# Performance work log

Measured on AMD Instinct MI355X. Metric: run time of the kernel, lower is better.

Reference implementation:

```python
import jax, jax.numpy as jnp
import numpy as np

DIM = 1024
NUM_HEADS = 16
HEAD_DIM = DIM // NUM_HEADS
SCALE = HEAD_DIM ** -0.5
B, N = 4, 2048


def setup_inputs() -> dict:
    key = jax.random.key(0)
    ks = jax.random.split(key, 8)
    s = DIM ** -0.5
    x = jax.random.normal(ks[0], (B, N, DIM), dtype=jnp.float32)
    mask = jax.random.randint(ks[1], (B, N, N), 0, 2, dtype=jnp.int32)
    wq = jax.random.normal(ks[2], (DIM, DIM), dtype=jnp.float32) * s
    wk = jax.random.normal(ks[3], (DIM, DIM), dtype=jnp.float32) * s
    wv = jax.random.normal(ks[4], (DIM, DIM), dtype=jnp.float32) * s
    wp = jax.random.normal(ks[5], (DIM, DIM), dtype=jnp.float32) * s
    bp = jnp.zeros((DIM,), dtype=jnp.float32)
    return {"x": x, "mask": mask, "wq": wq, "wk": wk, "wv": wv, "wp": wp, "bp": bp}


def reference(x, mask, wq, wk, wv, wp, bp):
    Bn, Nn, C = x.shape
    # torch Linear: y = x @ W^T; split heads -> (B, H, N, hd)
    def split_heads(y):
        return y.reshape(Bn, Nn, NUM_HEADS, HEAD_DIM).transpose(0, 2, 1, 3)
    q = split_heads(x @ wq.T)
    k = split_heads(x @ wk.T)
    v = split_heads(x @ wv.T)
    attn = jnp.einsum('bhqd,bhkd->bhqk', q, k) * SCALE  # (B,H,N,N)
    # mask==0 -> -inf; mask is (B,N,N), broadcast over heads
    attn = jnp.where(mask[:, None, :, :] == 0, -jnp.inf, attn)
    attn = jax.nn.softmax(attn, axis=-1)
    out = jnp.einsum('bhqk,bhkd->bhqd', attn, v)  # (B,H,N,hd)
    out = out.transpose(0, 2, 1, 3).reshape(Bn, Nn, C)
    return out @ wp.T + bp
```

## Files before the change

### kernel.cpp

```cpp
#include <hip/hip_runtime.h>
#include <stdint.h>

#define DIM 1024
#define NH 16
#define HD 64
#define BB 4
#define SS 2048
#define MR (BB*SS)
#define QSCALE 0.125f
#define L2E 1.44269504f

typedef float f32x4 __attribute__((ext_vector_type(4)));
typedef float f32x16 __attribute__((ext_vector_type(16)));
typedef __bf16 bf16x8 __attribute__((ext_vector_type(8)));
typedef uint32_t u32x4 __attribute__((ext_vector_type(4)));

typedef __attribute__((address_space(3))) void lds_void;
typedef __attribute__((address_space(1))) void glob_void;
#define GLL16(gp, lp) __builtin_amdgcn_global_load_lds((glob_void*)(gp), (lds_void*)(lp), 16, 0, 0)

static __device__ __forceinline__ ushort f2bf(float f) {
  uint32_t u = __builtin_bit_cast(uint32_t, f);
  u += 0x7FFF + ((u >> 16) & 1);
  return (ushort)(u >> 16);
}

static __device__ __forceinline__ f32x16 mfma32(bf16x8 a, bf16x8 b, f32x16 c) {
  return __builtin_amdgcn_mfma_f32_32x32x16_bf16(a, b, c, 0, 0, 0);
}
static __device__ __forceinline__ uint32_t cvtpk(float lo, float hi) {
  uint32_t r;
  asm("v_cvt_pk_bf16_f32 %0, %1, %2" : "=v"(r) : "v"(lo), "v"(hi));
  return r;
}
static __device__ __forceinline__ void plswap(uint32_t &a, uint32_t &b) {
  asm("v_permlane32_swap_b32 %0, %1" : "+v"(a), "+v"(b));
}

__global__ void cvt_bf16(const float* __restrict__ in, ushort* __restrict__ out,
                         const int n4) {
  const int stride = gridDim.x * blockDim.x;
  for (int i = blockIdx.x * blockDim.x + threadIdx.x; i < n4; i += stride) {
    const float4 v = reinterpret_cast<const float4*>(in)[i];
    ushort4 o;
    o.x = f2bf(v.x); o.y = f2bf(v.y); o.z = f2bf(v.z); o.w = f2bf(v.w);
    reinterpret_cast<ushort4*>(out)[i] = o;
  }
}

__global__ void cvt_w4(const float* __restrict__ w0, const float* __restrict__ w1,
                       const float* __restrict__ w2, const float* __restrict__ w3,
                       ushort* __restrict__ out) {
  const int n4 = DIM * DIM;
  const int rsz = DIM * DIM / 4;
  const int stride = gridDim.x * blockDim.x;
  for (int i = blockIdx.x * blockDim.x + threadIdx.x; i < n4; i += stride) {
    const int r = i / rsz, j = i - r * rsz;
    const float* src = (r == 0) ? w0 : (r == 1) ? w1 : (r == 2) ? w2 : w3;
    const float sc = (r == 0) ? (QSCALE * L2E) : 1.0f;
    const float4 v = reinterpret_cast<const float4*>(src)[j];
    ushort4 o;
    o.x = f2bf(v.x * sc); o.y = f2bf(v.y * sc);
    o.z = f2bf(v.z * sc); o.w = f2bf(v.w * sc);
    reinterpret_cast<ushort4*>(out)[i] = o;
  }
}

__global__ void pack_mask(const int* __restrict__ m, uint32_t* __restrict__ bits,
                          const int npairs) {
  const int lane = threadIdx.x & 63;
  const int wid = (blockIdx.x * blockDim.x + threadIdx.x) >> 6;
  const int nw = (gridDim.x * blockDim.x) >> 6;
  for (int p = wid; p < npairs; p += nw) {
    const int v = m[(size_t)p * 64 + lane];
    const unsigned long long bal = __ballot(v != 0);
    if (lane == 0) reinterpret_cast<unsigned long long*>(bits)[p] = bal;
  }
}

template<int EPI>
__global__ __launch_bounds__(256)
void gemm128(const ushort* __restrict__ A, const ushort* __restrict__ Bm,
             const int N, const int K,
             ushort* __restrict__ q_out, ushort* __restrict__ k_out,
             ushort* __restrict__ vt_out,
             const float* __restrict__ bias, float* __restrict__ c_out) {
  __shared__ __align__(16) ushort As[128 * 64];
  __shared__ __align__(16) ushort Bs[128 * 64];
  const int tid = threadIdx.x;
  const int lane = tid & 63, w = tid >> 6;
  const int l31 = lane & 31, hi = lane >> 5;
  const int gx = gridDim.x;
  int lin = blockIdx.y * gx + blockIdx.x;
  const int qch = (gx * gridDim.y) >> 3;
  lin = (lin & 7) * qch + (lin >> 3);
  const int tm = (lin / gx) * 128;
  const int tn = (lin % gx) * 128;
  const int wm = (w >> 1) * 64;
  const int wn = (w & 1) * 64;

  f32x16 acc[2][2] = {};

  const int srow = w * 32 + (lane >> 3);
  const int scol = ((lane & 7) ^ (lane >> 3)) * 8;
  const ushort* aptr = A + (size_t)(tm + srow) * K + scol;
  const ushort* bptr = Bm + (size_t)(tn + srow) * K + scol;
  ushort* lA = As + (size_t)(w * 32) * 64;
  ushort* lB = Bs + (size_t)(w * 32) * 64;

  const int swr = l31 & 7;

  for (int k0 = 0; k0 < K; k0 += 64) {
#pragma unroll
    for (int it = 0; it < 4; ++it) {
      GLL16(aptr + k0 + (size_t)(it * 8) * K, lA + it * 8 * 64);
      GLL16(bptr + k0 + (size_t)(it * 8) * K, lB + it * 8 * 64);
    }
    __syncthreads();
    bf16x8 af[4][2], bfr[4][2];
#pragma unroll
    for (int kk = 0; kk < 4; ++kk) {
      const int slot = (2 * kk + hi) ^ swr;
#pragma unroll
      for (int t = 0; t < 2; ++t) {
        af[kk][t]  = *reinterpret_cast<const bf16x8*>(As + (wm + t * 32 + l31) * 64 + slot * 8);
        bfr[kk][t] = *reinterpret_cast<const bf16x8*>(Bs + (wn + t * 32 + l31) * 64 + slot * 8);
      }
    }
#pragma unroll
    for (int kk = 0; kk < 4; ++kk)
#pragma unroll
      for (int ti = 0; ti < 2; ++ti)
#pragma unroll
        for (int tj = 0; tj < 2; ++tj)
          acc[ti][tj] = mfma32(af[kk][ti], bfr[kk][tj], acc[ti][tj]);
    __syncthreads();
  }

  if constexpr (EPI == 0) {
    const int which = tn >> 10;
    if (which < 2) {
      ushort* dst = which ? k_out : q_out;
#pragma unroll
      for (int ti = 0; ti < 2; ++ti)
#pragma unroll
        for (int tj = 0; tj < 2; ++tj) {
          const int cc = (tn + wn + tj * 32) & (DIM - 1);
          const int h = cc >> 6, d0 = cc & 63;
          const int mrb = tm + wm + ti * 32;
          const int bb = mrb >> 11, tokb = mrb & (SS - 1);
          const size_t bh = (size_t)bb * NH + h;
#pragma unroll
          for (int r = 0; r < 16; ++r) {
            const int tok = tokb + (r & 3) + 8 * (r >> 2) + 4 * hi;
            dst[(bh * SS + tok) * HD + d0 + l31] = f2bf(acc[ti][tj][r]);
          }
        }
    } else {
      ushort* ws = As + w * 1152;
#pragma unroll
      for (int ti = 0; ti < 2; ++ti)
#pragma unroll
        for (int tj = 0; tj < 2; ++tj) {
          const int cc = (tn + wn + tj * 32) & (DIM - 1);
          const int h = cc >> 6, d0 = cc & 63;
          const int mrb = tm + wm + ti * 32;
          const int bb = mrb >> 11, tokb = mrb & (SS - 1);
          const size_t bh = (size_t)bb * NH + h;
#pragma unroll
          for (int r = 0; r < 16; ++r)
            ws[l31 * 36 + (r & 3) + 8 * (r >> 2) + 4 * hi] = f2bf(acc[ti][tj][r]);
          asm volatile("s_waitcnt lgkmcnt(0)" ::: "memory");
          __builtin_amdgcn_sched_barrier(0);
#pragma unroll
          for (int p = 0; p < 8; ++p) {
            const int dl = p * 4 + (lane >> 4);
            const int tokl = (lane & 15) * 2;
            const uint32_t vv = *reinterpret_cast<const uint32_t*>(ws + dl * 36 + tokl);
            *reinterpret_cast<uint32_t*>(
                vt_out + (bh * HD + d0 + dl) * SS + tokb + tokl) = vv;
          }
          asm volatile("s_waitcnt lgkmcnt(0)" ::: "memory");
          __builtin_amdgcn_sched_barrier(0);
        }
    }
  } else {
#pragma unroll
    for (int ti = 0; ti < 2; ++ti)
#pragma unroll
      for (int tj = 0; tj < 2; ++tj) {
        const int nc = tn + wn + tj * 32 + l31;
#pragma unroll
        for (int r = 0; r < 16; ++r) {
          const int mrow = tm + wm + ti * 32 + (r & 3) + 8 * (r >> 2) + 4 * hi;
          c_out[(size_t)mrow * N + nc] = acc[ti][tj][r] + bias[nc];
        }
      }
  }
}

__global__ __launch_bounds__(512)
void attn_kernel(const ushort* __restrict__ Q, const ushort* __restrict__ Kg,
                 const ushort* __restrict__ Vt, const uint32_t* __restrict__ mb,
                 ushort* __restrict__ O) {
  __shared__ __align__(16) ushort lds[16384];
  __shared__ float rl_lds[8][32];

  const int tid = threadIdx.x, lane = tid & 63, w = tid >> 6;
  const int l31 = lane & 31, hi = lane >> 5;
  const int d = blockIdx.x;
  const int g = d & 63, m = d >> 6;
  const int h = g & 15, b = g >> 4;
  const size_t bh = (size_t)b * NH + h;
  const int q0w = m * 256 + w * 32;
  const int qg = q0w + l31;

  bf16x8 qf[4];
  const ushort* qp = Q + (bh * SS + qg) * HD + hi * 8;
#pragma unroll
  for (int kk = 0; kk < 4; ++kk)
    qf[kk] = *reinterpret_cast<const bf16x8*>(qp + kk * 16);

  f32x16 oacc[2] = {};
  float lrun = 0.f;

  const ushort* kbase = Kg + bh * SS * HD;
  const ushort* vbase = Vt + bh * HD * SS;
  const uint32_t* mrow = mb + ((size_t)b * SS + qg) * (SS / 32);

  auto stage = [&](int buf, int kv0) {
    GLL16(kbase + (size_t)(kv0 + (w >> 2) * 32 + l31) * HD + (w & 3) * 16 + hi * 8,
          lds + buf * 8192 + w * 512);
    GLL16(vbase + (size_t)((w & 1) * 32 + l31) * SS + kv0 + (w >> 1) * 16 + hi * 8,
          lds + buf * 8192 + 4096 + w * 512);
  };

  stage(0, 0);
  uint2 mw = *reinterpret_cast<const uint2*>(mrow);
  int cur = 0;

  for (int kv0 = 0; kv0 < SS; kv0 += 64) {
    __syncthreads();
    uint2 mw_n = mw;
    if (kv0 + 64 < SS) {
      stage(cur ^ 1, kv0 + 64);
      mw_n = *reinterpret_cast<const uint2*>(mrow + ((kv0 + 64) >> 5));
    }

    const ushort* kf = lds + cur * 8192 + lane * 8;
    const ushort* vf = lds + cur * 8192 + 4096 + lane * 8;

    f32x16 st[2];
    __builtin_amdgcn_s_setprio(1);
#pragma unroll
    for (int t = 0; t < 2; ++t) {
      f32x16 s = {};
#pragma unroll
      for (int kk = 0; kk < 4; ++kk) {
        const bf16x8 kfrag = *reinterpret_cast<const bf16x8*>(kf + (t * 4 + kk) * 512);
        s = mfma32(kfrag, qf[kk], s);
      }
      st[t] = s;
    }
    __builtin_amdgcn_s_setprio(0);

    float p[2][16];
#pragma unroll
    for (int t = 0; t < 2; ++t) {
      const uint32_t wts = (t ? mw.y : mw.x) >> (4 * hi);
#pragma unroll
      for (int r = 0; r < 16; ++r) {
        const int sh = (r & 3) + 8 * (r >> 2);
        const float pe = __builtin_amdgcn_exp2f(((wts >> sh) & 1u) ? st[t][r] : -3e38f);
        p[t][r] = pe;
        lrun += pe;
      }
    }

    bf16x8 PA[4];
#pragma unroll
    for (int t = 0; t < 2; ++t) {
      uint32_t pk[8];
#pragma unroll
      for (int i = 0; i < 8; ++i)
        pk[i] = cvtpk(p[t][2 * i], p[t][2 * i + 1]);
      plswap(pk[0], pk[2]);
      plswap(pk[1], pk[3]);
      plswap(pk[4], pk[6]);
      plswap(pk[5], pk[7]);
      const u32x4 lo = {pk[0], pk[1], pk[2], pk[3]};
      const u32x4 hh = {pk[4], pk[5], pk[6], pk[7]};
      PA[2 * t]     = __builtin_bit_cast(bf16x8, lo);
      PA[2 * t + 1] = __builtin_bit_cast(bf16x8, hh);
    }

    __builtin_amdgcn_s_setprio(1);
#pragma unroll
    for (int c = 0; c < 4; ++c)
#pragma unroll
      for (int dt = 0; dt < 2; ++dt) {
        const bf16x8 vfrag = *reinterpret_cast<const bf16x8*>(vf + (c * 2 + dt) * 512);
        oacc[dt] = mfma32(PA[c], vfrag, oacc[dt]);
      }
    __builtin_amdgcn_s_setprio(0);

    mw = mw_n;
    cur ^= 1;
  }

  lrun += __shfl_xor(lrun, 32, 64);
  const float rl = 1.0f / lrun;
  if (lane < 32) rl_lds[w][lane] = rl;
  asm volatile("s_waitcnt lgkmcnt(0)" ::: "memory");
  f32x4 rg[4];
#pragma unroll
  for (int g2 = 0; g2 < 4; ++g2)
    rg[g2] = *reinterpret_cast<const f32x4*>(&rl_lds[w][g2 * 8 + 4 * hi]);
#pragma unroll
  for (int dt = 0; dt < 2; ++dt)
#pragma unroll
    for (int r = 0; r < 16; ++r) {
      const int qrow = q0w + (r & 3) + 8 * (r >> 2) + 4 * hi;
      const float v = oacc[dt][r] * rg[r >> 2][r & 3];
      O[((size_t)b * SS + qrow) * DIM + h * HD + dt * 32 + l31] = f2bf(v);
    }
}

extern "C" void kernel_launch(void* const* d_in, const int* in_sizes, int n_in,
                              void* d_out, int out_size, void* d_ws, size_t ws_size,
                              hipStream_t stream) {
  const float* x  = (const float*)d_in[0];
  const int* mask = (const int*)d_in[1];
  const float* wq = (const float*)d_in[2];
  const float* wk = (const float*)d_in[3];
  const float* wv = (const float*)d_in[4];
  const float* wp = (const float*)d_in[5];
  const float* bp = (const float*)d_in[6];
  float* out = (float*)d_out;

  ushort* xb   = (ushort*)d_ws;
  ushort* wcat = xb + (size_t)MR * DIM;
  ushort* wpb  = wcat + (size_t)3 * DIM * DIM;
  ushort* Qb   = wpb + (size_t)DIM * DIM;
  ushort* Kb   = Qb + (size_t)MR * DIM;
  ushort* Vtb  = Kb + (size_t)MR * DIM;
  ushort* Ob   = Vtb + (size_t)MR * DIM;
  uint32_t* mb = (uint32_t*)(Ob + (size_t)MR * DIM);
  const size_t needed = ((size_t)MR * DIM * 5 + (size_t)4 * DIM * DIM) * 2 + (size_t)BB * SS * (SS / 8);
  if (ws_size < needed) return;

  cvt_bf16<<<2048, 256, 0, stream>>>(x, xb, MR * DIM / 4);
  cvt_w4<<<2048, 256, 0, stream>>>(wq, wk, wv, wp, wcat);
  pack_mask<<<2048, 256, 0, stream>>>(mask, mb, BB * SS * SS / 64);

  gemm128<0><<<dim3(3 * DIM / 128, MR / 128), 256, 0, stream>>>(
      xb, wcat, 3 * DIM, DIM, Qb, Kb, Vtb, nullptr, nullptr);

  attn_kernel<<<512, 512, 0, stream>>>(Qb, Kb, Vtb, mb, Ob);

  gemm128<1><<<dim3(DIM / 128, MR / 128), 256, 0, stream>>>(
      Ob, wpb, DIM, DIM, nullptr, nullptr, nullptr, bp, out);
}
```

Measured before the change: 217.1 us.

## Double KV tile to 128 per iteration and broadcast row sums via shuffles

The attention loop now stages 128 keys/values per iteration into a doubled LDS double-buffer and processes them in four 32-key sub-tiles, computing scores, softmax and PV per sub-tile. This halves the number of barriers and prefetch rounds and may interleave exp work with MFMAs better. The final normalization replaces the LDS round-trip with per-element __shfl broadcasts. The cost is doubled LDS use (64KB), which may reduce occupancy, and 32 extra shuffles in the epilogue.

```diff
diff --git a/kernel.cpp b/kernel.cpp
--- a/kernel.cpp
+++ b/kernel.cpp
@@ -203,8 +203,7 @@
 void attn_kernel(const ushort* __restrict__ Q, const ushort* __restrict__ Kg,
                  const ushort* __restrict__ Vt, const uint32_t* __restrict__ mb,
                  ushort* __restrict__ O) {
-  __shared__ __align__(16) ushort lds[16384];
-  __shared__ float rl_lds[8][32];
+  __shared__ __align__(16) ushort lds[32768];
 
   const int tid = threadIdx.x, lane = tid & 63, w = tid >> 6;
   const int l31 = lane & 31, hi = lane >> 5;
@@ -229,80 +228,80 @@
   const uint32_t* mrow = mb + ((size_t)b * SS + qg) * (SS / 32);
 
   auto stage = [&](int buf, int kv0) {
-    GLL16(kbase + (size_t)(kv0 + (w >> 2) * 32 + l31) * HD + (w & 3) * 16 + hi * 8,
-          lds + buf * 8192 + w * 512);
-    GLL16(vbase + (size_t)((w & 1) * 32 + l31) * SS + kv0 + (w >> 1) * 16 + hi * 8,
-          lds + buf * 8192 + 4096 + w * 512);
+#pragma unroll
+    for (int it = 0; it < 2; ++it) {
+      const int gg = w + it * 8;
+      GLL16(kbase + (size_t)(kv0 + (gg >> 2) * 32 + l31) * HD + (gg & 3) * 16 + hi * 8,
+            lds + buf * 16384 + gg * 512);
+      GLL16(vbase + (size_t)((gg & 1) * 32 + l31) * SS + kv0 + (gg >> 1) * 16 + hi * 8,
+            lds + buf * 16384 + 8192 + gg * 512);
+    }
   };
 
   stage(0, 0);
-  uint2 mw = *reinterpret_cast<const uint2*>(mrow);
+  uint4 mw = *reinterpret_cast<const uint4*>(mrow);
   int cur = 0;
 
-  for (int kv0 = 0; kv0 < SS; kv0 += 64) {
+  for (int kv0 = 0; kv0 < SS; kv0 += 128) {
     __syncthreads();
-    uint2 mw_n = mw;
-    if (kv0 + 64 < SS) {
-      stage(cur ^ 1, kv0 + 64);
-      mw_n = *reinterpret_cast<const uint2*>(mrow + ((kv0 + 64) >> 5));
-    }
-
-    const ushort* kf = lds + cur * 8192 + lane * 8;
-    const ushort* vf = lds + cur * 8192 + 4096 + lane * 8;
-
-    f32x16 st[2];
-    __builtin_amdgcn_s_setprio(1);
-#pragma unroll
-    for (int t = 0; t < 2; ++t) {
-      f32x16 s = {};
-#pragma unroll
-      for (int kk = 0; kk < 4; ++kk) {
-        const bf16x8 kfrag = *reinterpret_cast<const bf16x8*>(kf + (t * 4 + kk) * 512);
-        s = mfma32(kfrag, qf[kk], s);
-      }
-      st[t] = s;
-    }
-    __builtin_amdgcn_s_setprio(0);
-
-    float p[2][16];
-#pragma unroll
-    for (int t = 0; t < 2; ++t) {
-      const uint32_t wts = (t ? mw.y : mw.x) >> (4 * hi);
+    uint4 mw_n = mw;
+    if (kv0 + 128 < SS) {
+      stage(cur ^ 1, kv0 + 128);
+      mw_n = *reinterpret_cast<const uint4*>(mrow + ((kv0 + 128) >> 5));
+    }
+
+    const ushort* kf = lds + cur * 16384 + lane * 8;
+    const ushort* vf = lds + cur * 16384 + 8192 + lane * 8;
+    const uint32_t mwa[4] = {mw.x, mw.y, mw.z, mw.w};
+
+#pragma unroll
+    for (int t = 0; t < 4; ++t) {
+      f32x16 st;
+      {
+        f32x16 s = {};
+        __builtin_amdgcn_s_setprio(1);
+#pragma unroll
+        for (int kk = 0; kk < 4; ++kk) {
+          const bf16x8 kfrag = *reinterpret_cast<const bf16x8*>(kf + (t * 4 + kk) * 512);
+          s = mfma32(kfrag, qf[kk], s);
+        }
+        __builtin_amdgcn_s_setprio(0);
+        st = s;
+      }
+
+      float p[16];
+      const uint32_t wts = mwa[t] >> (4 * hi);
 #pragma unroll
       for (int r = 0; r < 16; ++r) {
         const int sh = (r & 3) + 8 * (r >> 2);
-        const float pe = __builtin_amdgcn_exp2f(((wts >> sh) & 1u) ? st[t][r] : -3e38f);
-        p[t][r] = pe;
+        const float pe = __builtin_amdgcn_exp2f(((wts >> sh) & 1u) ? st[r] : -3e38f);
+        p[r] = pe;
         lrun += pe;
       }
-    }
-
-    bf16x8 PA[4];
-#pragma unroll
-    for (int t = 0; t < 2; ++t) {
+
       uint32_t pk[8];
 #pragma unroll
       for (int i = 0; i < 8; ++i)
-        pk[i] = cvtpk(p[t][2 * i], p[t][2 * i + 1]);
+        pk[i] = cvtpk(p[2 * i], p[2 * i + 1]);
       plswap(pk[0], pk[2]);
       plswap(pk[1], pk[3]);
       plswap(pk[4], pk[6]);
       plswap(pk[5], pk[7]);
       const u32x4 lo = {pk[0], pk[1], pk[2], pk[3]};
       const u32x4 hh = {pk[4], pk[5], pk[6], pk[7]};
-      PA[2 * t]     = __builtin_bit_cast(bf16x8, lo);
-      PA[2 * t + 1] = __builtin_bit_cast(bf16x8, hh);
-    }
-
-    __builtin_amdgcn_s_setprio(1);
-#pragma unroll
-    for (int c = 0; c < 4; ++c)
+      const bf16x8 PA0 = __builtin_bit_cast(bf16x8, lo);
+      const bf16x8 PA1 = __builtin_bit_cast(bf16x8, hh);
+
+      __builtin_amdgcn_s_setprio(1);
 #pragma unroll
       for (int dt = 0; dt < 2; ++dt) {
-        const bf16x8 vfrag = *reinterpret_cast<const bf16x8*>(vf + (c * 2 + dt) * 512);
-        oacc[dt] = mfma32(PA[c], vfrag, oacc[dt]);
-      }
-    __builtin_amdgcn_s_setprio(0);
+        const bf16x8 v0 = *reinterpret_cast<const bf16x8*>(vf + ((2 * t) * 2 + dt) * 512);
+        const bf16x8 v1 = *reinterpret_cast<const bf16x8*>(vf + ((2 * t + 1) * 2 + dt) * 512);
+        oacc[dt] = mfma32(PA0, v0, oacc[dt]);
+        oacc[dt] = mfma32(PA1, v1, oacc[dt]);
+      }
+      __builtin_amdgcn_s_setprio(0);
+    }
 
     mw = mw_n;
     cur ^= 1;
@@ -310,18 +309,14 @@
 
   lrun += __shfl_xor(lrun, 32, 64);
   const float rl = 1.0f / lrun;
-  if (lane < 32) rl_lds[w][lane] = rl;
-  asm volatile("s_waitcnt lgkmcnt(0)" ::: "memory");
-  f32x4 rg[4];
-#pragma unroll
-  for (int g2 = 0; g2 < 4; ++g2)
-    rg[g2] = *reinterpret_cast<const f32x4*>(&rl_lds[w][g2 * 8 + 4 * hi]);
 #pragma unroll
   for (int dt = 0; dt < 2; ++dt)
 #pragma unroll
     for (int r = 0; r < 16; ++r) {
-      const int qrow = q0w + (r & 3) + 8 * (r >> 2) + 4 * hi;
-      const float v = oacc[dt][r] * rg[r >> 2][r & 3];
+      const int qi = (r & 3) + 8 * (r >> 2) + 4 * hi;
+      const float rls = __shfl(rl, qi, 64);
+      const int qrow = q0w + qi;
+      const float v = oacc[dt][r] * rls;
       O[((size_t)b * SS + qrow) * DIM + h * HD + dt * 32 + l31] = f2bf(v);
     }
 }
```

Result: faster. 208.1 us (-4.1%).
